# Optimization experiments

Measured on AMD Instinct MI355X. Metric: run time of the kernel, lower is better.

The kernel has to match this reference:

```python
import jax, jax.numpy as jnp
import numpy as np

TEMPERATURE = 0.5  # init temperature; attn_drop=0.0 so dropout is identity


def setup_inputs() -> dict:
    key = jax.random.key(0)
    k1, k2, k3 = jax.random.split(key, 3)
    B, H, N, D = 4, 8, 2048, 64
    q = jax.random.normal(k1, (B, H, N, D), dtype=jnp.float32)
    k = jax.random.normal(k2, (B, H, N, D), dtype=jnp.float32)
    v = jax.random.normal(k3, (B, H, N, D), dtype=jnp.float32)
    scale = jnp.asarray(D ** -0.5, dtype=jnp.float32)
    return {"q": q, "k": k, "v": v, "scale": scale}


def reference(q, k, v, scale):
    # logits: [B,H,N,N]
    logits = jnp.einsum("bhqd,bhkd->bhqk", q, k) * scale
    # first softmax acts as a soft mask over keys
    soft_mask = jax.nn.softmax(logits / TEMPERATURE, axis=-1)
    # second softmax over masked logits (elementwise product, NOT matmul)
    attn = jax.nn.softmax(logits * soft_mask, axis=-1)
    # dropout with p=0.0 is identity
    out = jnp.einsum("bhqk,bhkd->bhqd", attn, v)
    return out
```

## Files before the change

kernel.cpp:

```cpp
#include <hip/hip_runtime.h>


typedef _Float16 f16;
typedef f16 f16x8 __attribute__((ext_vector_type(8)));
typedef f16 f16x4 __attribute__((ext_vector_type(4)));
typedef float f32x4 __attribute__((ext_vector_type(4)));

#define MFMA32(a, b, c) __builtin_amdgcn_mfma_f32_16x16x32_f16((a), (b), (c), 0, 0, 0)
#define MFMA16(a, b, c) __builtin_amdgcn_mfma_f32_16x16x16f16((a), (b), (c), 0, 0, 0)
#define EXP2(x) __builtin_amdgcn_exp2f(x)

#define N_CTX 2048
#define DH 64
#define KT 64
#define NKT (N_CTX / KT)
#define ROWS 128
#define QS 72

#define C2 2.885390081777927f

__device__ inline unsigned pk(float a, float b) {
    typedef __fp16 fp16x2_t __attribute__((ext_vector_type(2)));
    union { fp16x2_t v; unsigned u; } x;
    x.v = __builtin_amdgcn_cvt_pkrtz(a, b);
    return x.u;
}

__global__ __launch_bounds__(512, 4)
void stk_attn_mfma(const float* __restrict__ qg, const float* __restrict__ kg,
                   const float* __restrict__ vglob, const float* __restrict__ sg,
                   float* __restrict__ og) {
    __shared__ f16 Ks[2][KT * QS];
    __shared__ f16 Vt[2][DH * QS];

    const int tid  = threadIdx.x;
    const int wv   = tid >> 6;
    const int lane = tid & 63;
    const int l15  = lane & 15;
    const int q4   = lane >> 4;
    const int vp   = tid & 31;
    const int vgr  = tid >> 5;
    const int bh   = blockIdx.x & 31;
    const int q0   = (blockIdx.x >> 5) * ROWS;
    const float scale2 = sg[0] * C2;

    const float* qb = qg + (size_t)bh * N_CTX * DH;
    const float* kb = kg + (size_t)bh * N_CTX * DH;
    const float* vb = vglob + (size_t)bh * N_CTX * DH;
    float*       ob = og + (size_t)bh * N_CTX * DH;

    f16x8 aq[2];
    {
        const float* qrow = qb + (size_t)(q0 + wv * 16 + l15) * DH;
        #pragma unroll
        for (int kc = 0; kc < 2; ++kc) {
            float4 a0 = *(const float4*)&qrow[kc * 32 + q4 * 8];
            float4 a1 = *(const float4*)&qrow[kc * 32 + q4 * 8 + 4];
            union { f16x8 h; unsigned u[4]; } A;
            A.u[0] = pk(a0.x * scale2, a0.y * scale2);
            A.u[1] = pk(a0.z * scale2, a0.w * scale2);
            A.u[2] = pk(a1.x * scale2, a1.y * scale2);
            A.u[3] = pk(a1.z * scale2, a1.w * scale2);
            aq[kc] = A.h;
        }
    }

    f16* const ks_w  = &Ks[0][0];
    const f16* const ks_r = &Ks[0][l15 * QS + q4 * 8];
    f16* const vt_w  = &Vt[0][(vgr * 4) * QS + 2 * vp];
    const f16* const vt_r = &Vt[0][l15 * QS + q4 * 4];
    const int KSB = KT * QS;

    float s1 = 0.f;
    float4 kr[2];
    #pragma unroll
    for (int it = 0; it < 2; ++it) {
        int idx = it * 512 + tid;
        kr[it] = *(const float4*)&kb[((size_t)(idx >> 4)) * DH + (idx & 15) * 4];
    }
    #pragma unroll
    for (int it = 0; it < 2; ++it) {
        int idx = it * 512 + tid;
        *(uint2*)&ks_w[(idx >> 4) * QS + (idx & 15) * 4] =
            make_uint2(pk(kr[it].x, kr[it].y), pk(kr[it].z, kr[it].w));
    }
    #pragma unroll
    for (int it = 0; it < 2; ++it) {
        int idx = it * 512 + tid;
        kr[it] = *(const float4*)&kb[((size_t)KT + (idx >> 4)) * DH + (idx & 15) * 4];
    }
    __syncthreads();

    for (int kt = 0; kt < NKT; ++kt) {
        const int cur = (kt & 1) * KSB, nxt = KSB - cur;
        #pragma unroll
        for (int it = 0; it < 2; ++it) {
            int idx = it * 512 + tid;
            *(uint2*)&ks_w[nxt + (idx >> 4) * QS + (idx & 15) * 4] =
                make_uint2(pk(kr[it].x, kr[it].y), pk(kr[it].z, kr[it].w));
        }
        {
            int tn = (kt + 2 < NKT) ? kt + 2 : NKT - 1;
            #pragma unroll
            for (int it = 0; it < 2; ++it) {
                int idx = it * 512 + tid;
                kr[it] = *(const float4*)&kb[((size_t)tn * KT + (idx >> 4)) * DH + (idx & 15) * 4];
            }
        }
        #pragma unroll
        for (int kgi = 0; kgi < 4; ++kgi) {
            f16x8 b0 = *(const f16x8*)&ks_r[cur + kgi * 16 * QS];
            f16x8 b1 = *(const f16x8*)&ks_r[cur + kgi * 16 * QS + 32];
            f32x4 acc = {0.f, 0.f, 0.f, 0.f};
            acc = MFMA32(b0, aq[0], acc);
            acc = MFMA32(b1, aq[1], acc);
            s1 += EXP2(acc[0]);
            s1 += EXP2(acc[1]);
            s1 += EXP2(acc[2]);
            s1 += EXP2(acc[3]);
        }
        __syncthreads();
    }
    s1 += __shfl_xor(s1, 16, 64);
    s1 += __shfl_xor(s1, 32, 64);
    const float inv1 = 0.5f / s1;

    float l2 = 0.f;
    f32x4 O[4];
    #pragma unroll
    for (int dt = 0; dt < 4; ++dt) O[dt] = (f32x4){0.f, 0.f, 0.f, 0.f};

    float4 vr[2];
    #pragma unroll
    for (int it = 0; it < 2; ++it) {
        int idx = it * 512 + tid;
        kr[it] = *(const float4*)&kb[((size_t)(idx >> 4)) * DH + (idx & 15) * 4];
    }
    #pragma unroll
    for (int it = 0; it < 2; ++it) {
        int idx = it * 512 + tid;
        *(uint2*)&ks_w[(idx >> 4) * QS + (idx & 15) * 4] =
            make_uint2(pk(kr[it].x, kr[it].y), pk(kr[it].z, kr[it].w));
    }
    {
        const float* vs = vb + ((size_t)2 * vp) * DH + vgr * 4;
        vr[0] = *(const float4*)(vs);
        vr[1] = *(const float4*)(vs + DH);
        #pragma unroll
        for (int j = 0; j < 4; ++j)
            *(unsigned*)&vt_w[j * QS] =
                pk(((const float*)&vr[0])[j], ((const float*)&vr[1])[j]);
        const float* vs1 = vb + ((size_t)KT + 2 * vp) * DH + vgr * 4;
        vr[0] = *(const float4*)(vs1);
        vr[1] = *(const float4*)(vs1 + DH);
    }
    #pragma unroll
    for (int it = 0; it < 2; ++it) {
        int idx = it * 512 + tid;
        kr[it] = *(const float4*)&kb[((size_t)KT + (idx >> 4)) * DH + (idx & 15) * 4];
    }
    __syncthreads();

    for (int kt = 0; kt < NKT; ++kt) {
        const int cur = (kt & 1) * KSB, nxt = KSB - cur;
        #pragma unroll
        for (int it = 0; it < 2; ++it) {
            int idx = it * 512 + tid;
            *(uint2*)&ks_w[nxt + (idx >> 4) * QS + (idx & 15) * 4] =
                make_uint2(pk(kr[it].x, kr[it].y), pk(kr[it].z, kr[it].w));
        }
        #pragma unroll
        for (int j = 0; j < 4; ++j)
            *(unsigned*)&vt_w[nxt + j * QS] =
                pk(((const float*)&vr[0])[j], ((const float*)&vr[1])[j]);
        f16x4 pfr[4];
        #pragma unroll
        for (int kgi = 0; kgi < 4; ++kgi) {
            f16x8 b0 = *(const f16x8*)&ks_r[cur + kgi * 16 * QS];
            f16x8 b1 = *(const f16x8*)&ks_r[cur + kgi * 16 * QS + 32];
            f32x4 acc = {0.f, 0.f, 0.f, 0.f};
            acc = MFMA32(b0, aq[0], acc);
            acc = MFMA32(b1, aq[1], acc);
            float e2r[4];
            #pragma unroll
            for (int r = 0; r < 4; ++r) {
                float a  = acc[r];
                float e1 = EXP2(a);
                float e2 = EXP2((a * e1) * inv1);
                l2 += e2;
                e2r[r] = e2;
            }
            union { f16x4 h; unsigned u[2]; } P;
            P.u[0] = pk(e2r[0], e2r[1]);
            P.u[1] = pk(e2r[2], e2r[3]);
            pfr[kgi] = P.h;
        }
        {
            int tn = (kt + 2 < NKT) ? kt + 2 : NKT - 1;
            #pragma unroll
            for (int it = 0; it < 2; ++it) {
                int idx = it * 512 + tid;
                kr[it] = *(const float4*)&kb[((size_t)tn * KT + (idx >> 4)) * DH + (idx & 15) * 4];
            }
            const float* vs = vb + ((size_t)tn * KT + 2 * vp) * DH + vgr * 4;
            vr[0] = *(const float4*)(vs);
            vr[1] = *(const float4*)(vs + DH);
        }
        #pragma unroll
        for (int kgi = 0; kgi < 4; ++kgi) {
            #pragma unroll
            for (int dt = 0; dt < 4; ++dt) {
                f16x4 av = *(const f16x4*)&vt_r[cur + dt * 16 * QS + kgi * 16];
                O[dt] = MFMA16(av, pfr[kgi], O[dt]);
            }
        }
        __syncthreads();
    }

    l2 += __shfl_xor(l2, 16, 64);
    l2 += __shfl_xor(l2, 32, 64);
    const float invl2 = 1.0f / l2;
    const size_t orow = (size_t)(q0 + wv * 16 + l15) * DH;
    #pragma unroll
    for (int dt = 0; dt < 4; ++dt) {
        float4 o;
        o.x = O[dt][0] * invl2;
        o.y = O[dt][1] * invl2;
        o.z = O[dt][2] * invl2;
        o.w = O[dt][3] * invl2;
        *(float4*)&ob[orow + dt * 16 + q4 * 4] = o;
    }
}

extern "C" void kernel_launch(void* const* d_in, const int* in_sizes, int n_in,
                              void* d_out, int out_size, void* d_ws, size_t ws_size,
                              hipStream_t stream) {
    const float* q = (const float*)d_in[0];
    const float* k = (const float*)d_in[1];
    const float* v = (const float*)d_in[2];
    const float* s = (const float*)d_in[3];
    float* out = (float*)d_out;
    dim3 grid(32 * 16);
    stk_attn_mfma<<<grid, 512, 0, stream>>>(q, k, v, s, out);
}
```

Before: 167.7 us.

## Process two 16-row query tiles per wave with 256-thread blocks

After: 171.9 us. +2.5%, slower.

```diff
diff --git a/kernel.cpp b/kernel.cpp
--- a/kernel.cpp
+++ b/kernel.cpp
@@ -26,7 +26,7 @@
     return x.u;
 }
 
-__global__ __launch_bounds__(512, 4)
+__global__ __launch_bounds__(256, 2)
 void stk_attn_mfma(const float* __restrict__ qg, const float* __restrict__ kg,
                    const float* __restrict__ vglob, const float* __restrict__ sg,
                    float* __restrict__ og) {
@@ -49,9 +49,10 @@
     const float* vb = vglob + (size_t)bh * N_CTX * DH;
     float*       ob = og + (size_t)bh * N_CTX * DH;
 
-    f16x8 aq[2];
-    {
-        const float* qrow = qb + (size_t)(q0 + wv * 16 + l15) * DH;
+    f16x8 aq[2][2];
+    #pragma unroll
+    for (int qc = 0; qc < 2; ++qc) {
+        const float* qrow = qb + (size_t)(q0 + wv * 32 + qc * 16 + l15) * DH;
         #pragma unroll
         for (int kc = 0; kc < 2; ++kc) {
             float4 a0 = *(const float4*)&qrow[kc * 32 + q4 * 8];
@@ -61,32 +62,32 @@
             A.u[1] = pk(a0.z * scale2, a0.w * scale2);
             A.u[2] = pk(a1.x * scale2, a1.y * scale2);
             A.u[3] = pk(a1.z * scale2, a1.w * scale2);
-            aq[kc] = A.h;
+            aq[qc][kc] = A.h;
         }
     }
 
     f16* const ks_w  = &Ks[0][0];
     const f16* const ks_r = &Ks[0][l15 * QS + q4 * 8];
-    f16* const vt_w  = &Vt[0][(vgr * 4) * QS + 2 * vp];
+    f16* const vt_w  = &Vt[0][(vgr * 8) * QS + 2 * vp];
     const f16* const vt_r = &Vt[0][l15 * QS + q4 * 4];
     const int KSB = KT * QS;
 
-    float s1 = 0.f;
-    float4 kr[2];
-    #pragma unroll
-    for (int it = 0; it < 2; ++it) {
-        int idx = it * 512 + tid;
+    float s1[2] = {0.f, 0.f};
+    float4 kr[4];
+    #pragma unroll
+    for (int it = 0; it < 4; ++it) {
+        int idx = it * 256 + tid;
         kr[it] = *(const float4*)&kb[((size_t)(idx >> 4)) * DH + (idx & 15) * 4];
     }
     #pragma unroll
-    for (int it = 0; it < 2; ++it) {
-        int idx = it * 512 + tid;
+    for (int it = 0; it < 4; ++it) {
+        int idx = it * 256 + tid;
         *(uint2*)&ks_w[(idx >> 4) * QS + (idx & 15) * 4] =
             make_uint2(pk(kr[it].x, kr[it].y), pk(kr[it].z, kr[it].w));
     }
     #pragma unroll
-    for (int it = 0; it < 2; ++it) {
-        int idx = it * 512 + tid;
+    for (int it = 0; it < 4; ++it) {
+        int idx = it * 256 + tid;
         kr[it] = *(const float4*)&kb[((size_t)KT + (idx >> 4)) * DH + (idx & 15) * 4];
     }
     __syncthreads();
@@ -94,16 +95,16 @@
     for (int kt = 0; kt < NKT; ++kt) {
         const int cur = (kt & 1) * KSB, nxt = KSB - cur;
         #pragma unroll
-        for (int it = 0; it < 2; ++it) {
-            int idx = it * 512 + tid;
+        for (int it = 0; it < 4; ++it) {
+            int idx = it * 256 + tid;
             *(uint2*)&ks_w[nxt + (idx >> 4) * QS + (idx & 15) * 4] =
                 make_uint2(pk(kr[it].x, kr[it].y), pk(kr[it].z, kr[it].w));
         }
         {
             int tn = (kt + 2 < NKT) ? kt + 2 : NKT - 1;
             #pragma unroll
-            for (int it = 0; it < 2; ++it) {
-                int idx = it * 512 + tid;
+            for (int it = 0; it < 4; ++it) {
+                int idx = it * 256 + tid;
                 kr[it] = *(const float4*)&kb[((size_t)tn * KT + (idx >> 4)) * DH + (idx & 15) * 4];
             }
         }
@@ -111,52 +112,67 @@
         for (int kgi = 0; kgi < 4; ++kgi) {
             f16x8 b0 = *(const f16x8*)&ks_r[cur + kgi * 16 * QS];
             f16x8 b1 = *(const f16x8*)&ks_r[cur + kgi * 16 * QS + 32];
-            f32x4 acc = {0.f, 0.f, 0.f, 0.f};
-            acc = MFMA32(b0, aq[0], acc);
-            acc = MFMA32(b1, aq[1], acc);
-            s1 += EXP2(acc[0]);
-            s1 += EXP2(acc[1]);
-            s1 += EXP2(acc[2]);
-            s1 += EXP2(acc[3]);
+            #pragma unroll
+            for (int qc = 0; qc < 2; ++qc) {
+                f32x4 acc = {0.f, 0.f, 0.f, 0.f};
+                acc = MFMA32(b0, aq[qc][0], acc);
+                acc = MFMA32(b1, aq[qc][1], acc);
+                s1[qc] += EXP2(acc[0]);
+                s1[qc] += EXP2(acc[1]);
+                s1[qc] += EXP2(acc[2]);
+                s1[qc] += EXP2(acc[3]);
+            }
         }
         __syncthreads();
     }
-    s1 += __shfl_xor(s1, 16, 64);
-    s1 += __shfl_xor(s1, 32, 64);
-    const float inv1 = 0.5f / s1;
-
-    float l2 = 0.f;
-    f32x4 O[4];
-    #pragma unroll
-    for (int dt = 0; dt < 4; ++dt) O[dt] = (f32x4){0.f, 0.f, 0.f, 0.f};
-
-    float4 vr[2];
-    #pragma unroll
-    for (int it = 0; it < 2; ++it) {
-        int idx = it * 512 + tid;
+    float inv1[2];
+    #pragma unroll
+    for (int qc = 0; qc < 2; ++qc) {
+        float v = s1[qc];
+        v += __shfl_xor(v, 16, 64);
+        v += __shfl_xor(v, 32, 64);
+        inv1[qc] = 0.5f / v;
+    }
+
+    float l2[2] = {0.f, 0.f};
+    f32x4 O[2][4];
+    #pragma unroll
+    for (int qc = 0; qc < 2; ++qc)
+        #pragma unroll
+        for (int dt = 0; dt < 4; ++dt) O[qc][dt] = (f32x4){0.f, 0.f, 0.f, 0.f};
+
+    float4 vr0, vr1, vr2, vr3;
+    #pragma unroll
+    for (int it = 0; it < 4; ++it) {
+        int idx = it * 256 + tid;
         kr[it] = *(const float4*)&kb[((size_t)(idx >> 4)) * DH + (idx & 15) * 4];
     }
     #pragma unroll
-    for (int it = 0; it < 2; ++it) {
-        int idx = it * 512 + tid;
+    for (int it = 0; it < 4; ++it) {
+        int idx = it * 256 + tid;
         *(uint2*)&ks_w[(idx >> 4) * QS + (idx & 15) * 4] =
             make_uint2(pk(kr[it].x, kr[it].y), pk(kr[it].z, kr[it].w));
     }
     {
-        const float* vs = vb + ((size_t)2 * vp) * DH + vgr * 4;
-        vr[0] = *(const float4*)(vs);
-        vr[1] = *(const float4*)(vs + DH);
-        #pragma unroll
-        for (int j = 0; j < 4; ++j)
-            *(unsigned*)&vt_w[j * QS] =
-                pk(((const float*)&vr[0])[j], ((const float*)&vr[1])[j]);
-        const float* vs1 = vb + ((size_t)KT + 2 * vp) * DH + vgr * 4;
-        vr[0] = *(const float4*)(vs1);
-        vr[1] = *(const float4*)(vs1 + DH);
-    }
-    #pragma unroll
-    for (int it = 0; it < 2; ++it) {
-        int idx = it * 512 + tid;
+        const float* vs = vb + ((size_t)(2 * vp)) * DH + vgr * 8;
+        float4 a0 = *(const float4*)(vs);
+        float4 a1 = *(const float4*)(vs + 4);
+        float4 b0 = *(const float4*)(vs + DH);
+        float4 b1 = *(const float4*)(vs + DH + 4);
+        #pragma unroll
+        for (int j = 0; j < 4; ++j) {
+            *(unsigned*)&vt_w[j * QS] = pk(((const float*)&a0)[j], ((const float*)&b0)[j]);
+            *(unsigned*)&vt_w[(4 + j) * QS] = pk(((const float*)&a1)[j], ((const float*)&b1)[j]);
+        }
+        const float* vs1 = vb + ((size_t)(KT + 2 * vp)) * DH + vgr * 8;
+        vr0 = *(const float4*)(vs1);
+        vr1 = *(const float4*)(vs1 + 4);
+        vr2 = *(const float4*)(vs1 + DH);
+        vr3 = *(const float4*)(vs1 + DH + 4);
+    }
+    #pragma unroll
+    for (int it = 0; it < 4; ++it) {
+        int idx = it * 256 + tid;
         kr[it] = *(const float4*)&kb[((size_t)KT + (idx >> 4)) * DH + (idx & 15) * 4];
     }
     __syncthreads();
@@ -164,71 +180,82 @@
     for (int kt = 0; kt < NKT; ++kt) {
         const int cur = (kt & 1) * KSB, nxt = KSB - cur;
         #pragma unroll
-        for (int it = 0; it < 2; ++it) {
-            int idx = it * 512 + tid;
+        for (int it = 0; it < 4; ++it) {
+            int idx = it * 256 + tid;
             *(uint2*)&ks_w[nxt + (idx >> 4) * QS + (idx & 15) * 4] =
                 make_uint2(pk(kr[it].x, kr[it].y), pk(kr[it].z, kr[it].w));
         }
         #pragma unroll
-        for (int j = 0; j < 4; ++j)
-            *(unsigned*)&vt_w[nxt + j * QS] =
-                pk(((const float*)&vr[0])[j], ((const float*)&vr[1])[j]);
-        f16x4 pfr[4];
+        for (int j = 0; j < 4; ++j) {
+            *(unsigned*)&vt_w[nxt + j * QS] = pk(((const float*)&vr0)[j], ((const float*)&vr2)[j]);
+            *(unsigned*)&vt_w[nxt + (4 + j) * QS] = pk(((const float*)&vr1)[j], ((const float*)&vr3)[j]);
+        }
+        f16x4 pfr[2][4];
         #pragma unroll
         for (int kgi = 0; kgi < 4; ++kgi) {
             f16x8 b0 = *(const f16x8*)&ks_r[cur + kgi * 16 * QS];
             f16x8 b1 = *(const f16x8*)&ks_r[cur + kgi * 16 * QS + 32];
-            f32x4 acc = {0.f, 0.f, 0.f, 0.f};
-            acc = MFMA32(b0, aq[0], acc);
-            acc = MFMA32(b1, aq[1], acc);
-            float e2r[4];
-            #pragma unroll
-            for (int r = 0; r < 4; ++r) {
-                float a  = acc[r];
-                float e1 = EXP2(a);
-                float e2 = EXP2((a * e1) * inv1);
-                l2 += e2;
-                e2r[r] = e2;
-            }
-            union { f16x4 h; unsigned u[2]; } P;
-            P.u[0] = pk(e2r[0], e2r[1]);
-            P.u[1] = pk(e2r[2], e2r[3]);
-            pfr[kgi] = P.h;
+            #pragma unroll
+            for (int qc = 0; qc < 2; ++qc) {
+                f32x4 acc = {0.f, 0.f, 0.f, 0.f};
+                acc = MFMA32(b0, aq[qc][0], acc);
+                acc = MFMA32(b1, aq[qc][1], acc);
+                float e2r[4];
+                #pragma unroll
+                for (int r = 0; r < 4; ++r) {
+                    float a  = acc[r];
+                    float e1 = EXP2(a);
+                    float e2 = EXP2((a * e1) * inv1[qc]);
+                    l2[qc] += e2;
+                    e2r[r] = e2;
+                }
+                union { f16x4 h; unsigned u[2]; } P;
+                P.u[0] = pk(e2r[0], e2r[1]);
+                P.u[1] = pk(e2r[2], e2r[3]);
+                pfr[qc][kgi] = P.h;
+            }
         }
         {
             int tn = (kt + 2 < NKT) ? kt + 2 : NKT - 1;
             #pragma unroll
-            for (int it = 0; it < 2; ++it) {
-                int idx = it * 512 + tid;
+            for (int it = 0; it < 4; ++it) {
+                int idx = it * 256 + tid;
                 kr[it] = *(const float4*)&kb[((size_t)tn * KT + (idx >> 4)) * DH + (idx & 15) * 4];
             }
-            const float* vs = vb + ((size_t)tn * KT + 2 * vp) * DH + vgr * 4;
-            vr[0] = *(const float4*)(vs);
-            vr[1] = *(const float4*)(vs + DH);
+            const float* vs = vb + ((size_t)tn * KT + 2 * vp) * DH + vgr * 8;
+            vr0 = *(const float4*)(vs);
+            vr1 = *(const float4*)(vs + 4);
+            vr2 = *(const float4*)(vs + DH);
+            vr3 = *(const float4*)(vs + DH + 4);
         }
         #pragma unroll
         for (int kgi = 0; kgi < 4; ++kgi) {
             #pragma unroll
             for (int dt = 0; dt < 4; ++dt) {
                 f16x4 av = *(const f16x4*)&vt_r[cur + dt * 16 * QS + kgi * 16];
-                O[dt] = MFMA16(av, pfr[kgi], O[dt]);
+                O[0][dt] = MFMA16(av, pfr[0][kgi], O[0][dt]);
+                O[1][dt] = MFMA16(av, pfr[1][kgi], O[1][dt]);
             }
         }
         __syncthreads();
     }
 
-    l2 += __shfl_xor(l2, 16, 64);
-    l2 += __shfl_xor(l2, 32, 64);
-    const float invl2 = 1.0f / l2;
-    const size_t orow = (size_t)(q0 + wv * 16 + l15) * DH;
-    #pragma unroll
-    for (int dt = 0; dt < 4; ++dt) {
-        float4 o;
-        o.x = O[dt][0] * invl2;
-        o.y = O[dt][1] * invl2;
-        o.z = O[dt][2] * invl2;
-        o.w = O[dt][3] * invl2;
-        *(float4*)&ob[orow + dt * 16 + q4 * 4] = o;
+    #pragma unroll
+    for (int qc = 0; qc < 2; ++qc) {
+        float v = l2[qc];
+        v += __shfl_xor(v, 16, 64);
+        v += __shfl_xor(v, 32, 64);
+        const float invl2 = 1.0f / v;
+        const size_t orow = (size_t)(q0 + wv * 32 + qc * 16 + l15) * DH;
+        #pragma unroll
+        for (int dt = 0; dt < 4; ++dt) {
+            float4 o;
+            o.x = O[qc][dt][0] * invl2;
+            o.y = O[qc][dt][1] * invl2;
+            o.z = O[qc][dt][2] * invl2;
+            o.w = O[qc][dt][3] * invl2;
+            *(float4*)&ob[orow + dt * 16 + q4 * 4] = o;
+        }
     }
 }
 
@@ -241,5 +268,5 @@
     const float* s = (const float*)d_in[3];
     float* out = (float*)d_out;
     dim3 grid(32 * 16);
-    stk_attn_mfma<<<grid, 512, 0, stream>>>(q, k, v, s, out);
+    stk_attn_mfma<<<grid, 256, 0, stream>>>(q, k, v, s, out);
 }
```
